# Optimization experiments

Measured on AMD Instinct MI355X. Metric: run time of the kernel, lower is better.

## Reference

```python
import jax, jax.numpy as jnp
import numpy as np

N = 100000      # nodes
E = 1600000     # edges (avg degree 16)
IN_C = 128
HID = 64
OUT_C = 2


def compute_norm(edge_index, n):
    """1/rowcount of M = I + A^T (distinct nonzeros per row, coalesce semantics)."""
    idt = edge_index.dtype
    ar = jnp.arange(n, dtype=idt)
    rows = jnp.concatenate([ar, edge_index[1]])  # M built from transposed edges
    cols = jnp.concatenate([ar, edge_index[0]])
    order = jnp.lexsort((cols, rows))
    rs, cs = rows[order], cols[order]
    uniq = jnp.concatenate([jnp.array([True]),
                            (rs[1:] != rs[:-1]) | (cs[1:] != cs[:-1])])
    rowcount = jnp.zeros((n,), jnp.float32).at[rs].add(uniq.astype(jnp.float32))
    return 1.0 / jnp.maximum(rowcount, 1.0)


def pan_conv(x, edge_index, w_lin, b_lin, w_pan, norm):
    # PyG PANConv, filter_size=1: out = diag(norm) @ (w0*I + w0*w1*A^T) @ (x W + b)
    h = x @ w_lin + b_lin                                   # [N, HID]
    src, dst = edge_index[0], edge_index[1]
    agg = jnp.zeros_like(h).at[dst].add(h[src])             # (A^T h)[i] = sum_{src->i} h[src]
    out = w_pan[0] * h + (w_pan[0] * w_pan[1]) * agg
    return norm[:, None] * out


def setup_inputs() -> dict:
    key = jax.random.key(0)
    ks = jax.random.split(key, 8)
    x = jax.random.normal(ks[0], (N, IN_C), jnp.float32)
    edge_index = jax.random.randint(ks[1], (2, E), 0, N, dtype=jnp.int32)
    w1_lin = jax.random.normal(ks[2], (IN_C, HID), jnp.float32) * 0.05
    b1_lin = jnp.zeros((HID,), jnp.float32)
    w1_pan = jax.random.uniform(ks[3], (2,), jnp.float32, 0.5, 1.5)
    w2_lin = jax.random.normal(ks[4], (HID, HID), jnp.float32) * 0.05
    b2_lin = jnp.zeros((HID,), jnp.float32)
    w2_pan = jax.random.uniform(ks[5], (2,), jnp.float32, 0.5, 1.5)
    wc = jax.random.normal(ks[6], (2 * HID, OUT_C), jnp.float32) * 0.05
    bc = jnp.zeros((OUT_C,), jnp.float32)
    return {"x": x, "edge_index": edge_index,
            "w1_lin": w1_lin, "b1_lin": b1_lin, "w1_pan": w1_pan,
            "w2_lin": w2_lin, "b2_lin": b2_lin, "w2_pan": w2_pan,
            "wc": wc, "bc": bc}


def reference(x, edge_index, w1_lin, b1_lin, w1_pan, w2_lin, b2_lin, w2_pan, wc, bc):
    n = x.shape[0]
    norm = compute_norm(edge_index, n)          # graph-structure only; shared by both layers
    h = pan_conv(x, edge_index, w1_lin, b1_lin, w1_pan, norm)
    h = jax.nn.relu(h)
    h = pan_conv(h, edge_index, w2_lin, b2_lin, w2_pan, norm)
    row, col = edge_index[0], edge_index[1]
    emb = jnp.concatenate([h[row], h[col]], axis=-1)  # [E, 2*HID]
    return emb @ wc + bc                               # [E, OUT_C]
```

## Files before the change

### kernel.cpp

```cpp
#include <hip/hip_runtime.h>
#include <hip/hip_bf16.h>

#define NNODES 100000
#define NEDGES 1600000
#define INC 128
#define HIDC 64
#define BSHIFT 8
#define NB ((NNODES + 255) / 256)
#define TILE 8192
#define HSLOTS 8192
#define CAP 8192
#define CAPE 8192
#define NBLK_FILL ((NEDGES + TILE - 1) / TILE)
#define NBLK_LIN ((NNODES + 63) / 64)

__device__ __forceinline__ float bf2f(unsigned short h) {
    return __uint_as_float((unsigned)h << 16);
}

__global__ __launch_bounds__(256) void fat_kernel(
        const float* __restrict__ x, const float* __restrict__ w,
        const float* __restrict__ b, unsigned short* __restrict__ out,
        const float* __restrict__ w2_lin, const float* __restrict__ b2,
        const float* __restrict__ wc, float* __restrict__ w44,
        float* __restrict__ bias4,
        const int* __restrict__ src, const int* __restrict__ dst,
        int* __restrict__ bucket_fill, unsigned int* __restrict__ staging) {
    __shared__ float xs[64][INC + 12];
    int t = threadIdx.x;
    if (blockIdx.x < NBLK_FILL) {
        int* cnt = (int*)&xs[0][0];
        int* basepos = cnt + NB;
        for (int i = t; i < NB; i += 256) cnt[i] = 0;
        __syncthreads();
        int tile0 = blockIdx.x * TILE;
        unsigned int sv[32];
        int meta[32];
#pragma unroll
        for (int i = 0; i < 32; i++) {
            int e = tile0 + i * 256 + t;
            meta[i] = -1;
            sv[i] = 0;
            if (e < NEDGES) {
                int s = src[e], d = dst[e];
                int bkt = d >> BSHIFT;
                int r = atomicAdd(&cnt[bkt], 1);
                meta[i] = (bkt << 13) | r;
                sv[i] = ((unsigned)(d & 255) << 17) | (unsigned)s;
            }
        }
        __syncthreads();
        for (int i = t; i < NB; i += 256) {
            int c = cnt[i];
            int g = (c > 0) ? atomicAdd(&bucket_fill[i], c) : 0;
            basepos[i] = (i << 13) + g;
        }
        __syncthreads();
#pragma unroll
        for (int i = 0; i < 32; i++) {
            if (meta[i] >= 0) {
                int bkt = meta[i] >> 13, r = meta[i] & 8191;
                staging[basepos[bkt] + r] = sv[i];
            }
        }
    } else {
        int node0 = (blockIdx.x - NBLK_FILL) * 64;
        int nn = min(64, NNODES - node0);
        constexpr int C4 = INC / 4;
        for (int idx = t; idx < 64 * C4; idx += 256) {
            int row = idx / C4, c4 = idx % C4;
            float4 v = make_float4(0.f, 0.f, 0.f, 0.f);
            if (row < nn) v = *(const float4*)(x + (size_t)(node0 + row) * INC + c4 * 4);
            *(float4*)(&xs[row][c4 * 4]) = v;
        }
        __syncthreads();
        int tn = t >> 4, tc = t & 15;
        int n0 = tn * 4, c0 = tc * 4;
        float4 bb = *(const float4*)(b + c0);
        float acc[4][4];
#pragma unroll
        for (int i = 0; i < 4; i++) {
            acc[i][0] = bb.x; acc[i][1] = bb.y; acc[i][2] = bb.z; acc[i][3] = bb.w;
        }
        float xr[4][4], wr[4][4], xn[4][4], wn[4][4];
#pragma unroll
        for (int i = 0; i < 4; i++)
            *(float4*)&xr[i][0] = *(const float4*)(&xs[n0 + i][0]);
#pragma unroll
        for (int j = 0; j < 4; j++)
            *(float4*)&wr[j][0] = *(const float4*)(w + (size_t)j * 64 + c0);
#pragma unroll 2
        for (int k = 0; k < INC; k += 4) {
            int kn = (k + 4 < INC) ? (k + 4) : 0;
#pragma unroll
            for (int i = 0; i < 4; i++)
                *(float4*)&xn[i][0] = *(const float4*)(&xs[n0 + i][kn]);
#pragma unroll
            for (int j = 0; j < 4; j++)
                *(float4*)&wn[j][0] = *(const float4*)(w + (size_t)(kn + j) * 64 + c0);
#pragma unroll
            for (int i = 0; i < 4; i++)
#pragma unroll
                for (int kk = 0; kk < 4; kk++)
#pragma unroll
                    for (int j = 0; j < 4; j++)
                        acc[i][j] += xr[i][kk] * wr[kk][j];
#pragma unroll
            for (int i = 0; i < 4; i++)
#pragma unroll
                for (int kk = 0; kk < 4; kk++) {
                    xr[i][kk] = xn[i][kk];
                    wr[i][kk] = wn[i][kk];
                }
        }
#pragma unroll
        for (int i = 0; i < 4; i++) {
            int node = node0 + n0 + i;
            if (node < NNODES) {
                __hip_bfloat16 h0 = __float2bfloat16(acc[i][0]);
                __hip_bfloat16 h1 = __float2bfloat16(acc[i][1]);
                __hip_bfloat16 h2 = __float2bfloat16(acc[i][2]);
                __hip_bfloat16 h3 = __float2bfloat16(acc[i][3]);
                ushort4 pk = make_ushort4(*(unsigned short*)&h0, *(unsigned short*)&h1,
                                          *(unsigned short*)&h2, *(unsigned short*)&h3);
                *(ushort4*)(out + (size_t)node * 64 + c0) = pk;
            }
        }
        if (blockIdx.x == NBLK_FILL) {
            if (t < 16)
                *(ushort4*)(out + (size_t)NNODES * 64 + t * 4) = make_ushort4(0, 0, 0, 0);
            int k = t >> 2, j = t & 3;
            float a = 0.0f;
#pragma unroll 8
            for (int i = 0; i < 64; i++) {
                float w4 = (j < 2) ? wc[i * 2 + j] : wc[(64 + i) * 2 + (j - 2)];
                a += w2_lin[k * 64 + i] * w4;
            }
            w44[k * 4 + j] = a;
            if (k == 0) {
                float bb4 = 0.0f;
                for (int i = 0; i < 64; i++) {
                    float w4 = (j < 2) ? wc[i * 2 + j] : wc[(64 + i) * 2 + (j - 2)];
                    bb4 += b2[i] * w4;
                }
                bias4[j] = bb4;
            }
        }
    }
}

__global__ __launch_bounds__(256) void fill2_kernel(
        const int* __restrict__ bucket_fill, const unsigned int* __restrict__ staging,
        int* __restrict__ csr_src, int* __restrict__ row_start,
        int* __restrict__ row_pdeg, float* __restrict__ norm, int n_nodes) {
    __shared__ int cnt[256];
    __shared__ int dcount[256];
    __shared__ int off[256];
    __shared__ int pscan[256];
    __shared__ unsigned short rank16[CAP];
    __shared__ unsigned int ht[HSLOTS];
    int t = threadIdx.x;
    int b = blockIdx.x;
    int node0 = b << BSHIFT;
    int nn = min(256, n_nodes - node0);
    cnt[t] = 0; dcount[t] = 0;
    {
        uint4* h4 = (uint4*)ht;
        uint4 ff = make_uint4(0xFFFFFFFFu, 0xFFFFFFFFu, 0xFFFFFFFFu, 0xFFFFFFFFu);
        for (int i = t; i < HSLOTS / 4; i += 256) h4[i] = ff;
    }
    __syncthreads();
    int start = b << 13;
    int total = bucket_fill[b];
    for (int li = t; li < total; li += 256) {
        unsigned int w = staging[start + li];
        int s = (int)(w & 0x1FFFFu);
        int dl = (int)(w >> 17);
        int r = atomicAdd(&cnt[dl], 1);
        rank16[li] = (unsigned short)r;
        if (s != node0 + dl) {
            unsigned int slot = ((w * 2654435761u) >> 13) & (HSLOTS - 1);
            while (true) {
                unsigned int prev = atomicCAS(&ht[slot], 0xFFFFFFFFu, w);
                if (prev == 0xFFFFFFFFu) { atomicAdd(&dcount[dl], 1); break; }
                if (prev == w) break;
                slot = (slot + 1) & (HSLOTS - 1);
            }
        }
    }
    __syncthreads();
    int cv = cnt[t];
    int pv = (cv + 7) & ~7;
    pscan[t] = pv;
    __syncthreads();
    for (int o = 1; o < 256; o <<= 1) {
        int xx = (t >= o) ? pscan[t - o] : 0;
        __syncthreads();
        pscan[t] += xx;
        __syncthreads();
    }
    off[t] = b * CAPE + pscan[t] - pv;
    __syncthreads();
    if (t < nn) {
        row_start[node0 + t] = off[t];
        row_pdeg[node0 + t] = pv;
        norm[node0 + t] = 1.0f / (1.0f + (float)dcount[t]);
    }
    for (int k = cv; k < pv; k++) csr_src[off[t] + k] = n_nodes;
    for (int li = t; li < total; li += 256) {
        unsigned int w = staging[start + li];
        int s = (int)(w & 0x1FFFFu);
        int dl = (int)(w >> 17);
        csr_src[off[dl] + (int)rank16[li]] = s;
    }
}

__global__ void agg_h_kernel(const unsigned int* __restrict__ lin32,
                             const int* __restrict__ row_start,
                             const int* __restrict__ row_pdeg,
                             const int* __restrict__ csr_src,
                             const float* __restrict__ norm,
                             const float* __restrict__ wpan, const float* __restrict__ w44,
                             const float* __restrict__ bias4, float* __restrict__ u,
                             int n_nodes) {
    int t = threadIdx.x;
    int node = blockIdx.x * 4 + (t >> 6);
    int lane = t & 63;
    int sl = lane & 31;
    int h5 = lane >> 5;
    if (blockIdx.x == 0 && t < 4) u[n_nodes * 4 + t] = 0.0f;
    if (node >= n_nodes) return;
    int e0 = row_start[node];
    int pd = row_pdeg[node];
    float aLo0 = 0.f, aHi0 = 0.f, aLo1 = 0.f, aHi1 = 0.f;
    for (int base = 0; base < pd; base += 64) {
        int sidx = csr_src[e0 + base + lane];
        int m = min(64, pd - base);
        for (int p = 0; p < m; p += 8) {
#pragma unroll
            for (int pp = 0; pp < 8; pp += 4) {
                int sA0 = __builtin_amdgcn_readlane(sidx, p + pp + 0);
                int sB0 = __builtin_amdgcn_readlane(sidx, p + pp + 1);
                int sA1 = __builtin_amdgcn_readlane(sidx, p + pp + 2);
                int sB1 = __builtin_amdgcn_readlane(sidx, p + pp + 3);
                int s0 = h5 ? sB0 : sA0;
                int s1 = h5 ? sB1 : sA1;
                unsigned int wd0 = lin32[(size_t)s0 * 32 + sl];
                unsigned int wd1 = lin32[(size_t)s1 * 32 + sl];
                aLo0 += __uint_as_float(wd0 << 16);
                aHi0 += __uint_as_float(wd0 & 0xFFFF0000u);
                aLo1 += __uint_as_float(wd1 << 16);
                aHi1 += __uint_as_float(wd1 & 0xFFFF0000u);
            }
        }
    }
    float accLo = aLo0 + aLo1;
    float accHi = aHi0 + aHi1;
    accLo += __shfl_xor(accLo, 32);
    accHi += __shfl_xor(accHi, 32);
    unsigned int wself = lin32[(size_t)node * 32 + sl];
    float nr = norm[node];
    float w0 = wpan[0];
    float w01 = wpan[0] * wpan[1];
    float vLo = fmaxf(nr * (w0 * __uint_as_float(wself << 16) + w01 * accLo), 0.0f);
    float vHi = fmaxf(nr * (w0 * __uint_as_float(wself & 0xFFFF0000u) + w01 * accHi), 0.0f);
    int c0 = 2 * sl;
    float4 wv0 = *(const float4*)(w44 + c0 * 4);
    float4 wv1 = *(const float4*)(w44 + (c0 + 1) * 4);
    float p0 = vLo * wv0.x + vHi * wv1.x;
    float p1 = vLo * wv0.y + vHi * wv1.y;
    float p2 = vLo * wv0.z + vHi * wv1.z;
    float p3 = vLo * wv0.w + vHi * wv1.w;
    for (int off = 16; off; off >>= 1) {
        p0 += __shfl_xor(p0, off);
        p1 += __shfl_xor(p1, off);
        p2 += __shfl_xor(p2, off);
        p3 += __shfl_xor(p3, off);
    }
    if (lane == 0) {
        float4 bb = *(const float4*)bias4;
        *(float4*)(u + node * 4) =
            make_float4(p0 + bb.x, p1 + bb.y, p2 + bb.z, p3 + bb.w);
    }
}

__global__ void agg_pq4_kernel(const float* __restrict__ u, const int* __restrict__ row_start,
                               const int* __restrict__ row_pdeg,
                               const int* __restrict__ csr_src,
                               const float* __restrict__ norm,
                               const float* __restrict__ wpan, float* __restrict__ pq,
                               int n_nodes) {
    int t = threadIdx.x;
    int node = blockIdx.x * 64 + (t >> 2);
    int j = t & 3;
    if (node >= n_nodes) return;
    int e0 = row_start[node];
    int pd = row_pdeg[node];
    float acc = 0.0f;
    for (int e = 0; e < pd; e += 8) {
#pragma unroll
        for (int k = 0; k < 8; k++) {
            int s = csr_src[e0 + e + k];
            acc += u[s * 4 + j];
        }
    }
    float w0 = wpan[0];
    float w01 = wpan[0] * wpan[1];
    pq[node * 4 + j] = norm[node] * (w0 * u[node * 4 + j] + w01 * acc);
}

__global__ void edge_out_kernel(const int* __restrict__ src, const int* __restrict__ dst,
                                const float* __restrict__ pq, const float* __restrict__ bc,
                                float* __restrict__ out, int n_edges) {
    int e = blockIdx.x * blockDim.x + threadIdx.x;
    if (e >= n_edges) return;
    int r = src[e], c = dst[e];
    float2 p = *(const float2*)(pq + r * 4);
    float2 q = *(const float2*)(pq + c * 4 + 2);
    float2 o = make_float2(p.x + q.x + bc[0], p.y + q.y + bc[1]);
    *(float2*)(out + e * 2) = o;
}

extern "C" void kernel_launch(void* const* d_in, const int* in_sizes, int n_in,
                              void* d_out, int out_size, void* d_ws, size_t ws_size,
                              hipStream_t stream) {
    const float* x      = (const float*)d_in[0];
    const int*   eidx   = (const int*)d_in[1];
    const float* w1_lin = (const float*)d_in[2];
    const float* b1_lin = (const float*)d_in[3];
    const float* w1_pan = (const float*)d_in[4];
    const float* w2_lin = (const float*)d_in[5];
    const float* b2_lin = (const float*)d_in[6];
    const float* w2_pan = (const float*)d_in[7];
    const float* wc     = (const float*)d_in[8];
    const float* bc     = (const float*)d_in[9];
    float* out = (float*)d_out;

    const int* src = eidx;
    const int* dst = eidx + NEDGES;

    char* ws = (char*)d_ws;
    size_t off = 0;
    auto carve = [&](size_t bytes) {
        char* p = ws + off;
        off = (off + bytes + 255) & ~(size_t)255;
        return p;
    };
    int*   bucket_fill = (int*)carve((size_t)NB * 4);
    int*   row_start = (int*)carve((size_t)NNODES * 4);
    int*   row_pdeg  = (int*)carve((size_t)NNODES * 4);
    unsigned int* staging = (unsigned int*)carve((size_t)NB * CAP * 4);
    int*   csr_src  = (int*)carve(((size_t)NB * CAPE + 256) * 4);
    float* nrm      = (float*)carve((size_t)NNODES * 4);
    unsigned short* bufA = (unsigned short*)carve((size_t)(NNODES + 1) * HIDC * 2);
    float* u        = (float*)carve((size_t)(NNODES + 1) * 4 * 4);
    float* pq       = (float*)carve((size_t)NNODES * 4 * 4);
    float* w44      = (float*)carve((size_t)64 * 4 * 4);
    float* bias4    = (float*)carve((size_t)4 * 4);
    (void)ws_size; (void)in_sizes; (void)n_in; (void)out_size;

    hipMemsetAsync(bucket_fill, 0, (size_t)NB * 4, stream);

    fat_kernel<<<NBLK_FILL + NBLK_LIN, 256, 0, stream>>>(
        x, w1_lin, b1_lin, bufA, w2_lin, b2_lin, wc, w44, bias4,
        src, dst, bucket_fill, staging);

    fill2_kernel<<<NB, 256, 0, stream>>>(bucket_fill, staging, csr_src, row_start, row_pdeg,
                                         nrm, NNODES);

    agg_h_kernel<<<(NNODES + 3) / 4, 256, 0, stream>>>(
        (const unsigned int*)bufA, row_start, row_pdeg, csr_src, nrm, w1_pan, w44, bias4,
        u, NNODES);

    agg_pq4_kernel<<<(NNODES + 63) / 64, 256, 0, stream>>>(
        u, row_start, row_pdeg, csr_src, nrm, w2_pan, pq, NNODES);

    edge_out_kernel<<<NEDGES / 256, 256, 0, stream>>>(src, dst, pq, bc, out, NEDGES);
}
```

Before: 256.6 us.

## Use split-bf16 MFMA for first-layer linear and move weight prep to separate kernel

Replaces the FP32 register-tiled x@W1 GEMM inside the fused kernel with MFMA 16x16x32 bf16 instructions, using a hi/lo bf16 split (three products) to keep near-FP32 accuracy. It adds a small pre-kernel that transposes and splits W1 into bf16 halves and computes the folded second-layer weights that were previously done in the fat kernel. Shared memory grows to two double bf16 tiles with XOR swizzling, and the edge-bucketing branch now stages packed values in LDS instead of registers. This costs an extra launch and more LDS per block, which may lower occupancy for the edge-fill blocks.

```diff
diff --git a/kernel.cpp b/kernel.cpp
--- a/kernel.cpp
+++ b/kernel.cpp
@@ -14,39 +14,79 @@
 #define NBLK_FILL ((NEDGES + TILE - 1) / TILE)
 #define NBLK_LIN ((NNODES + 63) / 64)
 
+typedef short bf16x8 __attribute__((ext_vector_type(8)));
+typedef float f32x4 __attribute__((ext_vector_type(4)));
+
 __device__ __forceinline__ float bf2f(unsigned short h) {
     return __uint_as_float((unsigned)h << 16);
 }
-
-__global__ __launch_bounds__(256) void fat_kernel(
-        const float* __restrict__ x, const float* __restrict__ w,
-        const float* __restrict__ b, unsigned short* __restrict__ out,
+__device__ __forceinline__ unsigned short f2bf(float f) {
+    __hip_bfloat16 h = __float2bfloat16(f);
+    return *(unsigned short*)&h;
+}
+
+__global__ __launch_bounds__(256) void prep_w_kernel(
+        const float* __restrict__ w1, unsigned short* __restrict__ wTh,
+        unsigned short* __restrict__ wTl,
         const float* __restrict__ w2_lin, const float* __restrict__ b2,
         const float* __restrict__ wc, float* __restrict__ w44,
-        float* __restrict__ bias4,
+        float* __restrict__ bias4, unsigned short* __restrict__ out) {
+    int t = threadIdx.x;
+    int e = blockIdx.x * 256 + t;
+    int c = e >> 7, k = e & 127;
+    float v = w1[k * 64 + c];
+    unsigned short hi = f2bf(v);
+    wTh[e] = hi;
+    wTl[e] = f2bf(v - bf2f(hi));
+    if (blockIdx.x == 0) {
+        if (t < 16)
+            *(ushort4*)(out + (size_t)NNODES * 64 + t * 4) = make_ushort4(0, 0, 0, 0);
+        int kk = t >> 2, j = t & 3;
+        float a = 0.0f;
+#pragma unroll 8
+        for (int i = 0; i < 64; i++) {
+            float w4 = (j < 2) ? wc[i * 2 + j] : wc[(64 + i) * 2 + (j - 2)];
+            a += w2_lin[kk * 64 + i] * w4;
+        }
+        w44[kk * 4 + j] = a;
+        if (kk == 0) {
+            float bb4 = 0.0f;
+            for (int i = 0; i < 64; i++) {
+                float w4 = (j < 2) ? wc[i * 2 + j] : wc[(64 + i) * 2 + (j - 2)];
+                bb4 += b2[i] * w4;
+            }
+            bias4[j] = bb4;
+        }
+    }
+}
+
+__global__ __launch_bounds__(256) void fat_kernel(
+        const float* __restrict__ x,
+        const unsigned short* __restrict__ wTh, const unsigned short* __restrict__ wTl,
+        const float* __restrict__ b, unsigned short* __restrict__ out,
         const int* __restrict__ src, const int* __restrict__ dst,
         int* __restrict__ bucket_fill, unsigned int* __restrict__ staging) {
-    __shared__ float xs[64][INC + 12];
+    __shared__ alignas(16) unsigned short s_a[2][64 * 128];
+    __shared__ alignas(16) unsigned short s_b[2][64 * 128];
     int t = threadIdx.x;
     if (blockIdx.x < NBLK_FILL) {
-        int* cnt = (int*)&xs[0][0];
+        int* cnt = (int*)&s_a[0][0];
         int* basepos = cnt + NB;
+        unsigned int* svl = (unsigned int*)&s_b[0][0];
         for (int i = t; i < NB; i += 256) cnt[i] = 0;
         __syncthreads();
         int tile0 = blockIdx.x * TILE;
-        unsigned int sv[32];
         int meta[32];
 #pragma unroll
         for (int i = 0; i < 32; i++) {
             int e = tile0 + i * 256 + t;
             meta[i] = -1;
-            sv[i] = 0;
             if (e < NEDGES) {
                 int s = src[e], d = dst[e];
                 int bkt = d >> BSHIFT;
                 int r = atomicAdd(&cnt[bkt], 1);
                 meta[i] = (bkt << 13) | r;
-                sv[i] = ((unsigned)(d & 255) << 17) | (unsigned)s;
+                svl[i * 256 + t] = ((unsigned)(d & 255) << 17) | (unsigned)s;
             }
         }
         __syncthreads();
@@ -60,90 +100,80 @@
         for (int i = 0; i < 32; i++) {
             if (meta[i] >= 0) {
                 int bkt = meta[i] >> 13, r = meta[i] & 8191;
-                staging[basepos[bkt] + r] = sv[i];
+                staging[basepos[bkt] + r] = svl[i * 256 + t];
             }
         }
     } else {
         int node0 = (blockIdx.x - NBLK_FILL) * 64;
-        int nn = min(64, NNODES - node0);
-        constexpr int C4 = INC / 4;
-        for (int idx = t; idx < 64 * C4; idx += 256) {
-            int row = idx / C4, c4 = idx % C4;
-            float4 v = make_float4(0.f, 0.f, 0.f, 0.f);
-            if (row < nn) v = *(const float4*)(x + (size_t)(node0 + row) * INC + c4 * 4);
-            *(float4*)(&xs[row][c4 * 4]) = v;
-        }
-        __syncthreads();
-        int tn = t >> 4, tc = t & 15;
-        int n0 = tn * 4, c0 = tc * 4;
-        float4 bb = *(const float4*)(b + c0);
-        float acc[4][4];
-#pragma unroll
-        for (int i = 0; i < 4; i++) {
-            acc[i][0] = bb.x; acc[i][1] = bb.y; acc[i][2] = bb.z; acc[i][3] = bb.w;
-        }
-        float xr[4][4], wr[4][4], xn[4][4], wn[4][4];
-#pragma unroll
-        for (int i = 0; i < 4; i++)
-            *(float4*)&xr[i][0] = *(const float4*)(&xs[n0 + i][0]);
-#pragma unroll
-        for (int j = 0; j < 4; j++)
-            *(float4*)&wr[j][0] = *(const float4*)(w + (size_t)j * 64 + c0);
-#pragma unroll 2
-        for (int k = 0; k < INC; k += 4) {
-            int kn = (k + 4 < INC) ? (k + 4) : 0;
-#pragma unroll
-            for (int i = 0; i < 4; i++)
-                *(float4*)&xn[i][0] = *(const float4*)(&xs[n0 + i][kn]);
-#pragma unroll
-            for (int j = 0; j < 4; j++)
-                *(float4*)&wn[j][0] = *(const float4*)(w + (size_t)(kn + j) * 64 + c0);
-#pragma unroll
-            for (int i = 0; i < 4; i++)
-#pragma unroll
-                for (int kk = 0; kk < 4; kk++)
-#pragma unroll
-                    for (int j = 0; j < 4; j++)
-                        acc[i][j] += xr[i][kk] * wr[kk][j];
-#pragma unroll
-            for (int i = 0; i < 4; i++)
-#pragma unroll
-                for (int kk = 0; kk < 4; kk++) {
-                    xr[i][kk] = xn[i][kk];
-                    wr[i][kk] = wn[i][kk];
-                }
-        }
-#pragma unroll
-        for (int i = 0; i < 4; i++) {
-            int node = node0 + n0 + i;
-            if (node < NNODES) {
-                __hip_bfloat16 h0 = __float2bfloat16(acc[i][0]);
-                __hip_bfloat16 h1 = __float2bfloat16(acc[i][1]);
-                __hip_bfloat16 h2 = __float2bfloat16(acc[i][2]);
-                __hip_bfloat16 h3 = __float2bfloat16(acc[i][3]);
-                ushort4 pk = make_ushort4(*(unsigned short*)&h0, *(unsigned short*)&h1,
-                                          *(unsigned short*)&h2, *(unsigned short*)&h3);
-                *(ushort4*)(out + (size_t)node * 64 + c0) = pk;
-            }
-        }
-        if (blockIdx.x == NBLK_FILL) {
-            if (t < 16)
-                *(ushort4*)(out + (size_t)NNODES * 64 + t * 4) = make_ushort4(0, 0, 0, 0);
-            int k = t >> 2, j = t & 3;
-            float a = 0.0f;
-#pragma unroll 8
-            for (int i = 0; i < 64; i++) {
-                float w4 = (j < 2) ? wc[i * 2 + j] : wc[(64 + i) * 2 + (j - 2)];
-                a += w2_lin[k * 64 + i] * w4;
-            }
-            w44[k * 4 + j] = a;
-            if (k == 0) {
-                float bb4 = 0.0f;
-                for (int i = 0; i < 64; i++) {
-                    float w4 = (j < 2) ? wc[i * 2 + j] : wc[(64 + i) * 2 + (j - 2)];
-                    bb4 += b2[i] * w4;
-                }
-                bias4[j] = bb4;
+        float4 vx[8];
+#pragma unroll
+        for (int it = 0; it < 8; it++) {
+            int idx = it * 256 + t;
+            int row = idx >> 5, c4 = idx & 31;
+            int node = node0 + row;
+            if (node < NNODES)
+                vx[it] = *(const float4*)(x + (size_t)node * INC + c4 * 4);
+            else
+                vx[it] = make_float4(0.f, 0.f, 0.f, 0.f);
+        }
+        uint4 vwh[4], vwl[4];
+#pragma unroll
+        for (int j = 0; j < 4; j++) {
+            vwh[j] = *(const uint4*)(wTh + (size_t)(j * 256 + t) * 8);
+            vwl[j] = *(const uint4*)(wTl + (size_t)(j * 256 + t) * 8);
+        }
+#pragma unroll
+        for (int it = 0; it < 8; it++) {
+            int idx = it * 256 + t;
+            int row = idx >> 5, c4 = idx & 31;
+            ushort4 hi, lo;
+            hi.x = f2bf(vx[it].x); lo.x = f2bf(vx[it].x - bf2f(hi.x));
+            hi.y = f2bf(vx[it].y); lo.y = f2bf(vx[it].y - bf2f(hi.y));
+            hi.z = f2bf(vx[it].z); lo.z = f2bf(vx[it].z - bf2f(hi.z));
+            hi.w = f2bf(vx[it].w); lo.w = f2bf(vx[it].w - bf2f(hi.w));
+            int ke = (c4 * 4) ^ ((row & 7) << 3);
+            *(ushort4*)&s_a[0][row * 128 + ke] = hi;
+            *(ushort4*)&s_a[1][row * 128 + ke] = lo;
+        }
+#pragma unroll
+        for (int j = 0; j < 4; j++) {
+            int idx = j * 256 + t;
+            int col = idx >> 4, k0 = (idx & 15) * 8;
+            int ke = k0 ^ ((col & 7) << 3);
+            *(uint4*)&s_b[0][col * 128 + ke] = vwh[j];
+            *(uint4*)&s_b[1][col * 128 + ke] = vwl[j];
+        }
+        __syncthreads();
+        int l = t & 63, wv = t >> 6;
+        int mr = l & 15, g = l >> 4;
+        int arow = wv * 16 + mr;
+        f32x4 acc[4] = {{0.f, 0.f, 0.f, 0.f}, {0.f, 0.f, 0.f, 0.f},
+                        {0.f, 0.f, 0.f, 0.f}, {0.f, 0.f, 0.f, 0.f}};
+#pragma unroll
+        for (int ks = 0; ks < 4; ks++) {
+            int k0 = ks * 32 + g * 8;
+            int ko = k0 ^ ((mr & 7) << 3);
+            bf16x8 ah = *(const bf16x8*)&s_a[0][arow * 128 + ko];
+            bf16x8 al = *(const bf16x8*)&s_a[1][arow * 128 + ko];
+#pragma unroll
+            for (int cb = 0; cb < 4; cb++) {
+                int bo = (cb * 16 + mr) * 128 + ko;
+                bf16x8 bh = *(const bf16x8*)&s_b[0][bo];
+                bf16x8 bl = *(const bf16x8*)&s_b[1][bo];
+                acc[cb] = __builtin_amdgcn_mfma_f32_16x16x32_bf16(ah, bh, acc[cb], 0, 0, 0);
+                acc[cb] = __builtin_amdgcn_mfma_f32_16x16x32_bf16(ah, bl, acc[cb], 0, 0, 0);
+                acc[cb] = __builtin_amdgcn_mfma_f32_16x16x32_bf16(al, bh, acc[cb], 0, 0, 0);
+            }
+        }
+#pragma unroll
+        for (int cb = 0; cb < 4; cb++) {
+            int col = cb * 16 + mr;
+            float bb = b[col];
+#pragma unroll
+            for (int r = 0; r < 4; r++) {
+                int node = node0 + wv * 16 + g * 4 + r;
+                if (node < NNODES)
+                    out[(size_t)node * 64 + col] = f2bf(acc[cb][r] + bb);
             }
         }
     }
@@ -357,13 +387,17 @@
     float* pq       = (float*)carve((size_t)NNODES * 4 * 4);
     float* w44      = (float*)carve((size_t)64 * 4 * 4);
     float* bias4    = (float*)carve((size_t)4 * 4);
+    unsigned short* wTh = (unsigned short*)carve((size_t)HIDC * INC * 2);
+    unsigned short* wTl = (unsigned short*)carve((size_t)HIDC * INC * 2);
     (void)ws_size; (void)in_sizes; (void)n_in; (void)out_size;
 
     hipMemsetAsync(bucket_fill, 0, (size_t)NB * 4, stream);
 
+    prep_w_kernel<<<32, 256, 0, stream>>>(w1_lin, wTh, wTl, w2_lin, b2_lin, wc,
+                                          w44, bias4, bufA);
+
     fat_kernel<<<NBLK_FILL + NBLK_LIN, 256, 0, stream>>>(
-        x, w1_lin, b1_lin, bufA, w2_lin, b2_lin, wc, w44, bias4,
-        src, dst, bucket_fill, staging);
+        x, wTh, wTl, b1_lin, bufA, src, dst, bucket_fill, staging);
 
     fill2_kernel<<<NB, 256, 0, stream>>>(bucket_fill, staging, csr_src, row_start, row_pdeg,
                                          nrm, NNODES);
```

Measured after the change: 249.2 us. -2.9%, faster.
